# Optimization experiments

Hardware: AMD Instinct MI355X
Metric: run time of the kernel (lower is better)

The kernel has to match this reference:

```python
import jax, jax.numpy as jnp
import numpy as np

N = 100000   # nodes
E = 1600000  # edges (avg degree 16)
F_IN, H1, H2, H3, C = 500, 200, 100, 40, 3


def setup_inputs() -> dict:
    key = jax.random.key(0)
    ks = jax.random.split(key, 10)
    def w(k, shape, fan_in):
        return jax.random.normal(k, shape, dtype=jnp.float32) / np.sqrt(fan_in)
    return {
        "x": jax.random.normal(ks[0], (N, F_IN), dtype=jnp.float32),
        "edge_index": jax.random.randint(ks[1], (2, E), 0, N, dtype=jnp.int32),
        "W1": w(ks[2], (H1, F_IN), F_IN), "b1": jnp.zeros((H1,), jnp.float32),
        "W1b": w(ks[3], (H2, H1), H1),  "b1b": jnp.zeros((H2,), jnp.float32),
        "W2b": w(ks[4], (H3, H2), H2),  "b2b": jnp.zeros((H3,), jnp.float32),
        "W2": w(ks[5], (C, H3), H3),    "b2": jnp.zeros((C,), jnp.float32),
    }


def _gcn_conv(x, W, b, src, dst, norm_e, n):
    # GCNConv: linear transform, then normalized scatter-add aggregation, then bias
    h = x @ W.T                                   # [N, out]
    msgs = h[src] * norm_e[:, None]               # [E+N, out] gathered, normalized
    out = jax.ops.segment_sum(msgs, dst, num_segments=n)
    return out + b


def reference(x, edge_index, W1, b1, W1b, b1b, W2b, b2b, W2, b2):
    n = x.shape[0]
    loop = jnp.arange(n, dtype=edge_index.dtype)
    src = jnp.concatenate([edge_index[0], loop])  # add self-loops (GCNConv default)
    dst = jnp.concatenate([edge_index[1], loop])
    # symmetric normalization: deg computed on target nodes, norm = d^-1/2[src]*d^-1/2[dst]
    deg = jax.ops.segment_sum(jnp.ones_like(dst, dtype=x.dtype), dst, num_segments=n)
    dinv = jnp.where(deg > 0, jax.lax.rsqrt(deg), 0.0)
    norm_e = dinv[src] * dinv[dst]

    # dropout(p=0.5, training=self.training) is identity at inference
    h = jax.nn.relu(_gcn_conv(x, W1, b1, src, dst, norm_e, n))
    h = jax.nn.relu(_gcn_conv(h, W1b, b1b, src, dst, norm_e, n))
    h = jax.nn.relu(_gcn_conv(h, W2b, b2b, src, dst, norm_e, n))
    return _gcn_conv(h, W2, b2, src, dst, norm_e, n)
```

## Files before the change

### kernel.cpp

```cpp
#include <hip/hip_runtime.h>


#define DEV __device__ __forceinline__

typedef __attribute__((ext_vector_type(8))) short short8;
typedef __attribute__((ext_vector_type(8))) _Float16 f16x8;
typedef __attribute__((ext_vector_type(4))) float f32x4;
typedef __attribute__((ext_vector_type(4))) _Float16 f16x4;

DEV void gload_lds16(const void* g, void* l) {
    __builtin_amdgcn_global_load_lds(
        (const __attribute__((address_space(1))) unsigned int*)g,
        (__attribute__((address_space(3))) unsigned int*)l, 16, 0, 0);
}


__global__ void k_prep(const int* __restrict__ dst, int* __restrict__ cnt,
                       int* __restrict__ rank, int E,
                       const float* __restrict__ W1, unsigned short* __restrict__ wh1,
                       const float* __restrict__ W1b, unsigned short* __restrict__ wh2,
                       unsigned short* __restrict__ wl2,
                       const float* __restrict__ W2b, unsigned short* __restrict__ wh3,
                       unsigned short* __restrict__ wl3) {
    const int SZ1 = 224 * 512, SZ2 = 128 * 256, SZ3 = 64 * 128;
    int i = blockIdx.x * 256 + threadIdx.x;
    if (i < E) {
        rank[i] = atomicAdd(&cnt[dst[i]], 1);
        return;
    }
    i -= E;
    if (i < SZ1) {
        int r = i >> 9, k = i & 511;
        float x = (r < 200 && k < 500) ? W1[r * 500 + k] : 0.f;
        wh1[i] = __builtin_bit_cast(unsigned short, (_Float16)x);
        return;
    }
    i -= SZ1;
    if (i < SZ2) {
        int r = i >> 8, k = i & 255;
        float x = (r < 100 && k < 200) ? W1b[r * 200 + k] : 0.f;
        _Float16 h = (_Float16)x;
        _Float16 l = (_Float16)((x - (float)h) * 2048.0f);
        wh2[i] = __builtin_bit_cast(unsigned short, h);
        wl2[i] = __builtin_bit_cast(unsigned short, l);
        return;
    }
    i -= SZ2;
    if (i < SZ3) {
        int r = i >> 7, k = i & 127;
        float x = (r < 40 && k < 100) ? W2b[r * 100 + k] : 0.f;
        _Float16 h = (_Float16)x;
        _Float16 l = (_Float16)((x - (float)h) * 2048.0f);
        wh3[i] = __builtin_bit_cast(unsigned short, h);
        wl3[i] = __builtin_bit_cast(unsigned short, l);
    }
}


__global__ void k_scan1(const int* __restrict__ cnt, int* __restrict__ row_start,
                        int* __restrict__ partial, float* __restrict__ dinv, int n) {
    __shared__ int sdata[256];
    int base = blockIdx.x * 1024;
    int t = threadIdx.x;
    int v[4]; int sum = 0;
#pragma unroll
    for (int j = 0; j < 4; ++j) {
        int idx = base + t * 4 + j;
        v[j] = (idx < n) ? (cnt[idx] + 1) : 0;
        if (idx < n) dinv[idx] = rsqrtf((float)v[j]);
        sum += v[j];
    }
    sdata[t] = sum;
    __syncthreads();
    for (int off = 1; off < 256; off <<= 1) {
        int x = (t >= off) ? sdata[t - off] : 0;
        __syncthreads();
        sdata[t] += x;
        __syncthreads();
    }
    int excl = sdata[t] - sum;
#pragma unroll
    for (int j = 0; j < 4; ++j) {
        int idx = base + t * 4 + j;
        if (idx < n) row_start[idx] = excl;
        excl += v[j];
    }
    if (t == 255) partial[blockIdx.x] = sdata[255];
}

__global__ void k_scan2(int* __restrict__ partial, int nb) {
    __shared__ int s[128];
    int t = threadIdx.x;
    int v = (t < nb) ? partial[t] : 0;
    s[t] = v;
    __syncthreads();
    for (int off = 1; off < 128; off <<= 1) {
        int x = (t >= off) ? s[t - off] : 0;
        __syncthreads();
        s[t] += x;
        __syncthreads();
    }
    if (t < nb) partial[t] = s[t] - v;
}

__global__ void k_scan3(int* __restrict__ row_start, const int* __restrict__ partial,
                        int n, int total) {
    int i = blockIdx.x * 256 + threadIdx.x;
    if (i < n) row_start[i] += partial[i >> 10];
    if (i == 0) row_start[n] = total;
}


struct A8 { f32x4 lo, hi; };

template <int NFC, int KPH, int NPH, int HILO, int MODE, int DOFILL, typename AT>
__global__ __launch_bounds__(512, 4)
void gemm_res(const AT* __restrict__ A, int lda, int M, int K,
              const unsigned short* __restrict__ Wh,
              const unsigned short* __restrict__ Wl,
              const float* __restrict__ dinv,
              _Float16* __restrict__ H16, int ldh, int Nout,
              const int* __restrict__ fsrc, const int* __restrict__ fdst,
              const int* __restrict__ frows, const int* __restrict__ fcnt,
              const int* __restrict__ frank, int* __restrict__ fcsr, int fE, int fN) {
    constexpr int NPAD = NFC * 16;
    constexpr int KP   = KPH * NPH;
    constexpr int CHH  = NPAD * KPH / 8;
    constexpr int CHT  = CHH * (1 + HILO);
    constexpr int NIT  = (CHT + 511) / 512;
    constexpr int SB   = NPAD * 64;
    constexpr int HB   = CHH * 16;
    constexpr int SPP  = KPH / 32;
    constexpr int NS   = SPP * NPH;
    constexpr int D    = 2;
    __shared__ char lds[CHT * 16];

    const int tid  = threadIdx.x;
    const int wv   = tid >> 6;
    const int lane = tid & 63;
    const int lr   = lane & 15;
    const int kq   = lane >> 4;
    const int m0   = blockIdx.y * 128;
    const int col0 = blockIdx.x * NPAD;

    if constexpr (DOFILL) {
        int total = fE + fN;
        int nb    = gridDim.y;
        int per   = (total + nb - 1) / nb;
        int base  = blockIdx.y * per;
        int end   = base + per; if (end > total) end = total;
        for (int i = base + tid; i < end; i += 512) {
            int s, pos;
            if (i < fE) {
                s = fsrc[i];
                pos = frows[fdst[i]] + frank[i];
            } else {
                s = i - fE;
                pos = frows[s] + fcnt[s];
            }
            fcsr[pos] = s;
        }
    }

    const unsigned short* WhB = Wh + (size_t)col0 * KP;
    const unsigned short* WlB = Wl + (size_t)col0 * KP;

    auto stageW = [&](int p) {
#pragma unroll
        for (int i = 0; i < NIT; ++i) {
            int c = tid + i * 512;
            if ((CHT % 512 == 0) || (c < CHT)) {
                int h  = (HILO && c >= CHH) ? 1 : 0;
                int cc = c - h * CHH;
                int st = cc / (NPAD * 4);
                int rm = cc - st * (NPAD * 4);
                int r  = rm >> 2;
                int sl = rm & 3;
                int gs = sl ^ (r & 3);
                const unsigned short* gp = (h ? WlB : WhB)
                    + (size_t)r * KP + p * KPH + st * 32 + gs * 8;
                gload_lds16(gp, lds + (size_t)c * 16);
            }
        }
    };

    int arow = m0 + wv * 16 + lr;
    if (arow >= M) arow = M - 1;
    const AT* Arow = A + (size_t)arow * lda;

    auto loadA32 = [&](int s) -> A8 {
        A8 o;
        int kb = s * 32 + kq * 8;
        if (kb + 8 <= K) {
            const float* ap = (const float*)Arow + kb;
            o.lo = *(const f32x4*)ap;
            o.hi = *(const f32x4*)(ap + 4);
        } else {
#pragma unroll
            for (int i = 0; i < 4; ++i) {
                int k0 = kb + i, k1 = kb + 4 + i;
                o.lo[i] = (k0 < K) ? (float)Arow[k0] : 0.f;
                o.hi[i] = (k1 < K) ? (float)Arow[k1] : 0.f;
            }
        }
        return o;
    };
    auto loadA16 = [&](int s) -> short8 {
        int kb = s * 32 + kq * 8;
        if (kb + 8 <= K) return *(const short8*)((const unsigned short*)Arow + kb);
        short8 o;
        const unsigned short* ap = (const unsigned short*)Arow;
#pragma unroll
        for (int i = 0; i < 8; ++i) o[i] = (kb + i < K) ? (short)ap[kb + i] : (short)0;
        return o;
    };
    auto cvtA = [&](const A8& a) -> f16x8 {
        f16x8 o;
#pragma unroll
        for (int i = 0; i < 4; ++i) {
            o[i]     = (_Float16)a.lo[i];
            o[4 + i] = (_Float16)a.hi[i];
        }
        return o;
    };

    stageW(0);
    A8 ab[D]; short8 hb[D];
#pragma unroll
    for (int p = 0; p < D; ++p) {
        if (p < NS) {
            if constexpr (MODE == 0) ab[p] = loadA32(p);
            else                     hb[p] = loadA16(p);
        }
    }

    f32x4 ac[NFC], al[NFC];
#pragma unroll
    for (int f = 0; f < NFC; ++f) {
        ac[f] = (f32x4){0.f, 0.f, 0.f, 0.f};
        al[f] = (f32x4){0.f, 0.f, 0.f, 0.f};
    }

    __syncthreads();

    const int ro = lr * 64 + ((kq ^ (lr & 3)) << 4);

#pragma unroll
    for (int p = 0; p < NPH; ++p) {
#pragma unroll
        for (int sl = 0; sl < SPP; ++sl) {
            const int s = p * SPP + sl;
            f16x8 a0;
            if constexpr (MODE == 0) a0 = cvtA(ab[s % D]);
            else                     a0 = __builtin_bit_cast(f16x8, hb[s % D]);

            if (s + D < NS) {
                if constexpr (MODE == 0) ab[s % D] = loadA32(s + D);
                else                     hb[s % D] = loadA16(s + D);
            }

            const char* bb = lds + sl * SB;
#pragma unroll
            for (int f = 0; f < NFC; ++f) {
                f16x8 bh = __builtin_bit_cast(f16x8, *(const short8*)(bb + f * 1024 + ro));
                ac[f] = __builtin_amdgcn_mfma_f32_16x16x32_f16(a0, bh, ac[f], 0, 0, 0);
                if constexpr (HILO) {
                    f16x8 bl = __builtin_bit_cast(f16x8, *(const short8*)(bb + HB + f * 1024 + ro));
                    al[f] = __builtin_amdgcn_mfma_f32_16x16x32_f16(a0, bl, al[f], 0, 0, 0);
                }
            }
        }
        if (p + 1 < NPH) {
            __syncthreads();
            stageW(p + 1);
            __syncthreads();
        }
    }

    const int rbase = m0 + wv * 16 + kq * 4;
    float dv[4];
#pragma unroll
    for (int j = 0; j < 4; ++j) {
        int row = rbase + j;
        dv[j] = (row < M) ? dinv[row] : 0.f;
    }
#pragma unroll
    for (int f = 0; f < NFC; ++f) {
        int col = col0 + f * 16 + lr;
        if (col >= Nout) continue;
#pragma unroll
        for (int j = 0; j < 4; ++j) {
            int row = rbase + j;
            if (row >= M) continue;
            float v = ac[f][j];
            if constexpr (HILO) v += al[f][j] * (1.0f / 2048.0f);
            H16[(size_t)row * ldh + col] = (_Float16)(v * dv[j]);
        }
    }
}


template <int F, int VEC, bool RELU>
__global__ __launch_bounds__(256)
void agg_f16(const _Float16* __restrict__ h, const int* __restrict__ row_start,
             const int* __restrict__ csr_src, const float* __restrict__ dinv,
             const float* __restrict__ bias, _Float16* __restrict__ out, int n,
             int ldo) {
    constexpr int LPN = F / VEC;
    constexpr int NPW = 64 / LPN;
    int wave = blockIdx.x * 4 + (threadIdx.x >> 6);
    int lane = threadIdx.x & 63;
    int sub  = lane / LPN;
    int fi   = lane - sub * LPN;
    int node = wave * NPW + sub;
    if (sub >= NPW || node >= n) return;
    int f = fi * VEC;
    const _Float16* hf = h + f;

    f32x4 acc0 = {0.f, 0.f, 0.f, 0.f};
    f32x4 acc1 = {0.f, 0.f, 0.f, 0.f};

    auto addv = [&](const _Float16* p) {
        if constexpr (VEC == 8) {
            f16x8 v = *(const f16x8*)p;
            f16x4 vl, vh;
#pragma unroll
            for (int j = 0; j < 4; ++j) { vl[j] = v[j]; vh[j] = v[4 + j]; }
            acc0 += __builtin_convertvector(vl, f32x4);
            acc1 += __builtin_convertvector(vh, f32x4);
        } else {
            f16x4 v = *(const f16x4*)p;
            acc0 += __builtin_convertvector(v, f32x4);
        }
    };

    int e0 = row_start[node], e1 = row_start[node + 1];
    int e = e0;
    for (; e + 8 <= e1; e += 8) {
        int s0 = csr_src[e + 0], s1 = csr_src[e + 1];
        int s2 = csr_src[e + 2], s3 = csr_src[e + 3];
        int s4 = csr_src[e + 4], s5 = csr_src[e + 5];
        int s6 = csr_src[e + 6], s7 = csr_src[e + 7];
        const _Float16* p0 = &hf[(size_t)s0 * F];
        const _Float16* p1 = &hf[(size_t)s1 * F];
        const _Float16* p2 = &hf[(size_t)s2 * F];
        const _Float16* p3 = &hf[(size_t)s3 * F];
        const _Float16* p4 = &hf[(size_t)s4 * F];
        const _Float16* p5 = &hf[(size_t)s5 * F];
        const _Float16* p6 = &hf[(size_t)s6 * F];
        const _Float16* p7 = &hf[(size_t)s7 * F];
        addv(p0); addv(p1); addv(p2); addv(p3);
        addv(p4); addv(p5); addv(p6); addv(p7);
    }
    for (; e + 4 <= e1; e += 4) {
        int s0 = csr_src[e + 0], s1 = csr_src[e + 1];
        int s2 = csr_src[e + 2], s3 = csr_src[e + 3];
        const _Float16* p0 = &hf[(size_t)s0 * F];
        const _Float16* p1 = &hf[(size_t)s1 * F];
        const _Float16* p2 = &hf[(size_t)s2 * F];
        const _Float16* p3 = &hf[(size_t)s3 * F];
        addv(p0); addv(p1); addv(p2); addv(p3);
    }
    for (; e < e1; ++e) addv(&hf[(size_t)csr_src[e] * F]);

    float dn = dinv[node];
    if constexpr (VEC == 8) {
        f32x4 b0 = *(const f32x4*)&bias[f];
        f32x4 b1 = *(const f32x4*)&bias[f + 4];
        acc0 = acc0 * dn + b0;
        acc1 = acc1 * dn + b1;
        if (RELU) {
#pragma unroll
            for (int j = 0; j < 4; ++j) { acc0[j] = fmaxf(acc0[j], 0.f); acc1[j] = fmaxf(acc1[j], 0.f); }
        }
        f16x8 o;
#pragma unroll
        for (int j = 0; j < 4; ++j) { o[j] = (_Float16)acc0[j]; o[4 + j] = (_Float16)acc1[j]; }
        *(f16x8*)&out[(size_t)node * ldo + f] = o;
    } else {
        f32x4 b4 = *(const f32x4*)&bias[f];
        acc0 = acc0 * dn + b4;
        if (RELU) {
#pragma unroll
            for (int j = 0; j < 4; ++j) acc0[j] = fmaxf(acc0[j], 0.f);
        }
        f16x4 o;
#pragma unroll
        for (int j = 0; j < 4; ++j) o[j] = (_Float16)acc0[j];
        *(f16x4*)&out[(size_t)node * ldo + f] = o;
    }
}


__global__ void gemm_small(const _Float16* __restrict__ A, const float* __restrict__ B,
                           const float* __restrict__ dinv, float* __restrict__ C,
                           int M, int K) {
    int m = blockIdx.x * 256 + threadIdx.x;
    if (m >= M) return;
    float a0 = 0.f, a1 = 0.f, a2 = 0.f;
    for (int k = 0; k < K; ++k) {
        float a = (float)A[(size_t)m * K + k];
        a0 += a * B[0 * K + k];
        a1 += a * B[1 * K + k];
        a2 += a * B[2 * K + k];
    }
    float dv = dinv[m];
    C[(size_t)m * 3 + 0] = a0 * dv;
    C[(size_t)m * 3 + 1] = a1 * dv;
    C[(size_t)m * 3 + 2] = a2 * dv;
}

__global__ void agg_f3(const float* __restrict__ h, const int* __restrict__ row_start,
                       const int* __restrict__ csr_src, const float* __restrict__ dinv,
                       const float* __restrict__ bias, float* __restrict__ out, int n) {
    int i = blockIdx.x * 256 + threadIdx.x;
    if (i >= n * 3) return;
    int node = i / 3;
    int f = i - node * 3;
    float acc = 0.f;
    int e1 = row_start[node + 1];
    for (int e = row_start[node]; e < e1; ++e) {
        int s = csr_src[e];
        acc += h[(size_t)s * 3 + f];
    }
    out[i] = acc * dinv[node] + bias[f];
}


extern "C" void kernel_launch(void* const* d_in, const int* in_sizes, int n_in,
                              void* d_out, int out_size, void* d_ws, size_t ws_size,
                              hipStream_t stream) {
    const float* x   = (const float*)d_in[0];
    const int*   ei  = (const int*)d_in[1];
    const float* W1  = (const float*)d_in[2];
    const float* b1  = (const float*)d_in[3];
    const float* W1b = (const float*)d_in[4];
    const float* b1b = (const float*)d_in[5];
    const float* W2b = (const float*)d_in[6];
    const float* b2b = (const float*)d_in[7];
    const float* W2  = (const float*)d_in[8];
    const float* b2  = (const float*)d_in[9];
    float* out = (float*)d_out;

    const int F_IN = 500, H1 = 200, H2 = 100, H3 = 40;
    const int N = in_sizes[0] / F_IN;
    const int E = in_sizes[1] / 2;
    const int* src = ei;
    const int* dst = ei + E;

    size_t off = 0;
    auto alloc = [&](size_t bytes) -> void* {
        void* p = (char*)d_ws + off;
        off += (bytes + 255) & ~(size_t)255;
        return p;
    };
    int*   cnt       = (int*)  alloc((size_t)N * 4);
    int*   row_start = (int*)  alloc((size_t)(N + 1) * 4);
    int*   rank      = (int*)  alloc((size_t)E * 4);
    int*   partial   = (int*)  alloc(128 * 4);
    float* dinv      = (float*)alloc((size_t)N * 4);
    int*   csr_src   = (int*)  alloc((size_t)(E + N) * 4);
    unsigned short* wh1 = (unsigned short*)alloc(224 * 512 * 2);
    unsigned short* wh2 = (unsigned short*)alloc(128 * 256 * 2);
    unsigned short* wl2 = (unsigned short*)alloc(128 * 256 * 2);
    unsigned short* wh3 = (unsigned short*)alloc( 64 * 128 * 2);
    unsigned short* wl3 = (unsigned short*)alloc( 64 * 128 * 2);
    _Float16* h16   = (_Float16*)alloc((size_t)N * H1 * 2);
    _Float16* act16 = (_Float16*)alloc((size_t)N * H1 * 2);
    float*    bufC  = (float*)   alloc((size_t)N * 3 * 4);

    int gN = (N + 255) / 256;
    int nb = (N + 1023) / 1024;

    hipMemsetAsync(cnt, 0, (size_t)N * 4, stream);
    {
        int total = E + 224 * 512 + 128 * 256 + 64 * 128;
        k_prep<<<(total + 255) / 256, 256, 0, stream>>>(dst, cnt, rank, E,
                                                        W1, wh1, W1b, wh2, wl2,
                                                        W2b, wh3, wl3);
    }
    k_scan1<<<nb, 256, 0, stream>>>(cnt, row_start, partial, dinv, N);
    k_scan2<<<1, 128, 0, stream>>>(partial, nb);
    k_scan3<<<gN, 256, 0, stream>>>(row_start, partial, N, E + N);

    const int gR = (N + 127) / 128;

    gemm_res<14, 128, 4, 0, 0, 1, float><<<dim3(1, gR), 512, 0, stream>>>(
        x, F_IN, N, F_IN, wh1, wh1, dinv, h16, H1, H1,
        src, dst, row_start, cnt, rank, csr_src, E, N);
    {
        int waves = (N + 1) / 2, blocks = (waves + 3) / 4;
        agg_f16<200, 8, true><<<blocks, 256, 0, stream>>>(h16, row_start, csr_src, dinv,
                                                          b1, act16, N, 200);
    }
    gemm_res<4, 128, 2, 1, 1, 0, _Float16><<<dim3(2, gR), 512, 0, stream>>>(
        act16, 200, N, H1, wh2, wl2, dinv, h16, H2, H2,
        nullptr, nullptr, nullptr, nullptr, nullptr, nullptr, 0, 0);
    agg_f16<100, 4, true><<<(N / 2 + 3) / 4, 256, 0, stream>>>(h16, row_start, csr_src, dinv,
                                                               b1b, act16, N, 112);
    gemm_res<4, 128, 1, 1, 1, 0, _Float16><<<dim3(1, gR), 512, 0, stream>>>(
        act16, 112, N, H2, wh3, wl3, dinv, h16, H3, H3,
        nullptr, nullptr, nullptr, nullptr, nullptr, nullptr, 0, 0);
    {
        int waves = (N + 11) / 12, blocks = (waves + 3) / 4;
        agg_f16<40, 8, true><<<blocks, 256, 0, stream>>>(h16, row_start, csr_src, dinv,
                                                         b2b, act16, N, 40);
    }
    gemm_small<<<(N + 255) / 256, 256, 0, stream>>>(act16, W2, dinv, bufC, N, H3);
    agg_f3<<<(N * 3 + 255) / 256, 256, 0, stream>>>(bufC, row_start, csr_src, dinv,
                                                    b2, out, N);
}
```

Baseline: 490.2 us.

## Store GEMM outputs in 16-column chunked layout for cache-friendly aggregation

The first two GEMMs now write their fp16 output in a column-chunked layout ([col/16][row][16]), padded to 208 and 112 columns. A new aggregation kernel handles one 16-wide chunk per grid-y slice, so each gather pass reads from a table of 3.2 MB or less that can stay cache-resident instead of striding through the full feature rows. This trades the CSR index reads, which now repeat once per chunk (13 or 7 times), plus extra padding writes, for better locality in the random gathers.

New measurement: 594.3 us. +21.2%, slower.

```diff
diff --git a/kernel.cpp b/kernel.cpp
--- a/kernel.cpp
+++ b/kernel.cpp
@@ -113,7 +113,8 @@
 
 struct A8 { f32x4 lo, hi; };
 
-template <int NFC, int KPH, int NPH, int HILO, int MODE, int DOFILL, typename AT>
+template <int NFC, int KPH, int NPH, int HILO, int MODE, int DOFILL, int CHUNKED,
+          typename AT>
 __global__ __launch_bounds__(512, 4)
 void gemm_res(const AT* __restrict__ A, int lda, int M, int K,
               const unsigned short* __restrict__ Wh,
@@ -294,9 +295,84 @@
             if (row >= M) continue;
             float v = ac[f][j];
             if constexpr (HILO) v += al[f][j] * (1.0f / 2048.0f);
-            H16[(size_t)row * ldh + col] = (_Float16)(v * dv[j]);
-        }
-    }
+            _Float16 o = (_Float16)(v * dv[j]);
+            if constexpr (CHUNKED)
+                H16[((size_t)(col >> 4) * M + row) * 16 + (col & 15)] = o;
+            else
+                H16[(size_t)row * ldh + col] = o;
+        }
+    }
+}
+
+
+template <int F, int F2, bool RELU>
+__global__ __launch_bounds__(256)
+void agg_ch(const _Float16* __restrict__ h, const int* __restrict__ row_start,
+            const int* __restrict__ csr_src, const float* __restrict__ dinv,
+            const float* __restrict__ bias, _Float16* __restrict__ out, int n) {
+    int gid  = blockIdx.x * 256 + threadIdx.x;
+    int node = gid >> 1;
+    int fi   = gid & 1;
+    if (node >= n) return;
+    int chunk = blockIdx.y;
+    const _Float16* tb = h + (size_t)chunk * n * 16 + fi * 8;
+    int fg = chunk * 16 + fi * 8;
+
+    f32x4 acc0 = {0.f, 0.f, 0.f, 0.f};
+    f32x4 acc1 = {0.f, 0.f, 0.f, 0.f};
+
+    auto addv = [&](const _Float16* p) {
+        f16x8 v = *(const f16x8*)p;
+        f16x4 vl, vh;
+#pragma unroll
+        for (int j = 0; j < 4; ++j) { vl[j] = v[j]; vh[j] = v[4 + j]; }
+        acc0 += __builtin_convertvector(vl, f32x4);
+        acc1 += __builtin_convertvector(vh, f32x4);
+    };
+
+    int e0 = row_start[node], e1 = row_start[node + 1];
+    int e = e0;
+    for (; e + 8 <= e1; e += 8) {
+        int s0 = csr_src[e + 0], s1 = csr_src[e + 1];
+        int s2 = csr_src[e + 2], s3 = csr_src[e + 3];
+        int s4 = csr_src[e + 4], s5 = csr_src[e + 5];
+        int s6 = csr_src[e + 6], s7 = csr_src[e + 7];
+        const _Float16* p0 = &tb[(size_t)s0 * 16];
+        const _Float16* p1 = &tb[(size_t)s1 * 16];
+        const _Float16* p2 = &tb[(size_t)s2 * 16];
+        const _Float16* p3 = &tb[(size_t)s3 * 16];
+        const _Float16* p4 = &tb[(size_t)s4 * 16];
+        const _Float16* p5 = &tb[(size_t)s5 * 16];
+        const _Float16* p6 = &tb[(size_t)s6 * 16];
+        const _Float16* p7 = &tb[(size_t)s7 * 16];
+        addv(p0); addv(p1); addv(p2); addv(p3);
+        addv(p4); addv(p5); addv(p6); addv(p7);
+    }
+    for (; e + 4 <= e1; e += 4) {
+        int s0 = csr_src[e + 0], s1 = csr_src[e + 1];
+        int s2 = csr_src[e + 2], s3 = csr_src[e + 3];
+        const _Float16* p0 = &tb[(size_t)s0 * 16];
+        const _Float16* p1 = &tb[(size_t)s1 * 16];
+        const _Float16* p2 = &tb[(size_t)s2 * 16];
+        const _Float16* p3 = &tb[(size_t)s3 * 16];
+        addv(p0); addv(p1); addv(p2); addv(p3);
+    }
+    for (; e < e1; ++e) addv(&tb[(size_t)csr_src[e] * 16]);
+
+    float dn = dinv[node];
+    float bv[8];
+#pragma unroll
+    for (int j = 0; j < 8; ++j) bv[j] = (fg + j < F) ? bias[fg + j] : 0.f;
+    f16x8 o;
+#pragma unroll
+    for (int j = 0; j < 4; ++j) {
+        float v0 = acc0[j] * dn + bv[j];
+        float v1 = acc1[j] * dn + bv[4 + j];
+        if (RELU) { v0 = fmaxf(v0, 0.f); v1 = fmaxf(v1, 0.f); }
+        o[j] = (_Float16)v0;
+        o[4 + j] = (_Float16)v1;
+    }
+    *(f16x8*)&out[(size_t)node * F2 + fg] = o;
 }
 
 
@@ -341,25 +417,16 @@
         int s2 = csr_src[e + 2], s3 = csr_src[e + 3];
         int s4 = csr_src[e + 4], s5 = csr_src[e + 5];
         int s6 = csr_src[e + 6], s7 = csr_src[e + 7];
-        const _Float16* p0 = &hf[(size_t)s0 * F];
-        const _Float16* p1 = &hf[(size_t)s1 * F];
-        const _Float16* p2 = &hf[(size_t)s2 * F];
-        const _Float16* p3 = &hf[(size_t)s3 * F];
-        const _Float16* p4 = &hf[(size_t)s4 * F];
-        const _Float16* p5 = &hf[(size_t)s5 * F];
-        const _Float16* p6 = &hf[(size_t)s6 * F];
-        const _Float16* p7 = &hf[(size_t)s7 * F];
-        addv(p0); addv(p1); addv(p2); addv(p3);
-        addv(p4); addv(p5); addv(p6); addv(p7);
+        addv(&hf[(size_t)s0 * F]); addv(&hf[(size_t)s1 * F]);
+        addv(&hf[(size_t)s2 * F]); addv(&hf[(size_t)s3 * F]);
+        addv(&hf[(size_t)s4 * F]); addv(&hf[(size_t)s5 * F]);
+        addv(&hf[(size_t)s6 * F]); addv(&hf[(size_t)s7 * F]);
     }
     for (; e + 4 <= e1; e += 4) {
         int s0 = csr_src[e + 0], s1 = csr_src[e + 1];
         int s2 = csr_src[e + 2], s3 = csr_src[e + 3];
-        const _Float16* p0 = &hf[(size_t)s0 * F];
-        const _Float16* p1 = &hf[(size_t)s1 * F];
-        const _Float16* p2 = &hf[(size_t)s2 * F];
-        const _Float16* p3 = &hf[(size_t)s3 * F];
-        addv(p0); addv(p1); addv(p2); addv(p3);
+        addv(&hf[(size_t)s0 * F]); addv(&hf[(size_t)s1 * F]);
+        addv(&hf[(size_t)s2 * F]); addv(&hf[(size_t)s3 * F]);
     }
     for (; e < e1; ++e) addv(&hf[(size_t)csr_src[e] * F]);
 
@@ -465,8 +532,8 @@
     unsigned short* wl2 = (unsigned short*)alloc(128 * 256 * 2);
     unsigned short* wh3 = (unsigned short*)alloc( 64 * 128 * 2);
     unsigned short* wl3 = (unsigned short*)alloc( 64 * 128 * 2);
-    _Float16* h16   = (_Float16*)alloc((size_t)N * H1 * 2);
-    _Float16* act16 = (_Float16*)alloc((size_t)N * H1 * 2);
+    _Float16* h16   = (_Float16*)alloc((size_t)N * 208 * 2);
+    _Float16* act16 = (_Float16*)alloc((size_t)N * 208 * 2);
     float*    bufC  = (float*)   alloc((size_t)N * 3 * 4);
 
     int gN = (N + 255) / 256;
@@ -484,22 +551,20 @@
     k_scan3<<<gN, 256, 0, stream>>>(row_start, partial, N, E + N);
 
     const int gR = (N + 127) / 128;
-
-    gemm_res<14, 128, 4, 0, 0, 1, float><<<dim3(1, gR), 512, 0, stream>>>(
-        x, F_IN, N, F_IN, wh1, wh1, dinv, h16, H1, H1,
+    const int gA = (2 * N + 255) / 256;
+
+    gemm_res<14, 128, 4, 0, 0, 1, 1, float><<<dim3(1, gR), 512, 0, stream>>>(
+        x, F_IN, N, F_IN, wh1, wh1, dinv, h16, 0, 208,
         src, dst, row_start, cnt, rank, csr_src, E, N);
-    {
-        int waves = (N + 1) / 2, blocks = (waves + 3) / 4;
-        agg_f16<200, 8, true><<<blocks, 256, 0, stream>>>(h16, row_start, csr_src, dinv,
-                                                          b1, act16, N, 200);
-    }
-    gemm_res<4, 128, 2, 1, 1, 0, _Float16><<<dim3(2, gR), 512, 0, stream>>>(
-        act16, 200, N, H1, wh2, wl2, dinv, h16, H2, H2,
+    agg_ch<200, 208, true><<<dim3(gA, 13), 256, 0, stream>>>(
+        h16, row_start, csr_src, dinv, b1, act16, N);
+    gemm_res<4, 128, 2, 1, 1, 0, 1, _Float16><<<dim3(2, gR), 512, 0, stream>>>(
+        act16, 208, N, H1, wh2, wl2, dinv, h16, 0, 112,
         nullptr, nullptr, nullptr, nullptr, nullptr, nullptr, 0, 0);
-    agg_f16<100, 4, true><<<(N / 2 + 3) / 4, 256, 0, stream>>>(h16, row_start, csr_src, dinv,
-                                                               b1b, act16, N, 112);
-    gemm_res<4, 128, 1, 1, 1, 0, _Float16><<<dim3(1, gR), 512, 0, stream>>>(
-        act16, 112, N, H2, wh3, wl3, dinv, h16, H3, H3,
+    agg_ch<100, 112, true><<<dim3(gA, 7), 256, 0, stream>>>(
+        h16, row_start, csr_src, dinv, b1b, act16, N);
+    gemm_res<4, 128, 1, 1, 1, 0, 0, _Float16><<<dim3(1, gR), 512, 0, stream>>>(
+        act16, 112, N, H2, wh3, wl3, dinv, h16, 40, 40,
         nullptr, nullptr, nullptr, nullptr, nullptr, nullptr, 0, 0);
     {
         int waves = (N + 11) / 12, blocks = (waves + 3) / 4;
```
